# Kernel tuning notes

Hardware: AMD Instinct MI355X
Metric: run time of the kernel (lower is better)

Reference implementation:

```python
import jax, jax.numpy as jnp
import numpy as np

B, N, C, E = 512, 1000, 50, 128
H, D = 8, 16          # head_num, qkv_dim; H*D == E
CLIP = 10.0           # logit_clipping
NEG = -1e9


def setup_inputs() -> dict:
    key = jax.random.key(0)
    ks = jax.random.split(key, 20)
    f = lambda i, shape, s=1.0: jax.random.normal(ks[i], shape, dtype=jnp.float32) * s
    w = 0.05  # small weight scale so tanh/softmax stay in a sane range
    return dict(
        depot_embedding=f(0, (B, 1, E)),
        cluster_embedding=f(1, (B, C, E)),
        current_embedding=f(2, (B, 1, E)),
        node_embeddings=f(3, (B, N, E)),
        aug_context_embedding=f(4, (B, 1, 4 * E)),
        cluster_guidance_embedding=f(5, (B, 1, E)),
        Wq=f(6, (3 * E, E), w), Wk=f(7, (E, E), w), Wv=f(8, (E, E), w), Wks=f(9, (E, E), w),
        mha_Wq=f(10, (E, H * D), w), mha_Wk=f(11, (E, H * D), w),
        mha_Wv=f(12, (E, H * D), w), mha_Wo=f(13, (H * D, E), w),
        is_new_cluster=jax.random.bernoulli(ks[14], 0.5, (B,)),
        mask=jax.random.bernoulli(ks[15], 0.5, (B, 1, N)),
        cluster_mask=jax.random.bernoulli(ks[16], 0.5, (B, 1, N)),
        visited_cluster_mask=jax.random.bernoulli(ks[17], 0.3, (B, 1, C)),
        cluster_guidance=jax.random.randint(ks[18], (B,), 0, C),
        step=1,
    )


def reference(depot_embedding, cluster_embedding, current_embedding, node_embeddings,
              aug_context_embedding, cluster_guidance_embedding,
              Wq, Wk, Wv, Wks, mha_Wq, mha_Wk, mha_Wv, mha_Wo,
              is_new_cluster, mask, cluster_mask, visited_cluster_mask,
              cluster_guidance, step):
    # step > 0 path: init_* buffers come from the passed-in tensors.
    b, n, e = node_embeddings.shape
    c = cluster_embedding.shape[1]

    def unvisit_embed(m):  # m: [B,1,N] bool, True = visited
        mm = m[:, 0, :, None]                                    # [B,N,1]
        return jnp.where(mm, 0.0, node_embeddings).sum(axis=1, keepdims=True) / n  # [B,1,E]

    # --- new-cluster branch, computed full-batch and selected with where ---
    unvisit_mean = unvisit_embed(mask)                            # [B,1,E]
    context = jnp.concatenate([unvisit_mean, current_embedding, depot_embedding], axis=2)  # [B,1,3E]
    q = context @ Wq                                              # [B,1,E]
    k = cluster_embedding @ Wk                                    # [B,C,E]
    v = cluster_embedding @ Wv                                    # [B,C,E]
    pk = cluster_embedding @ Wks                                  # [B,C,E]

    # if all non-depot clusters visited, unmask cluster 0; else mask it
    all_visited = jnp.all(visited_cluster_mask[:, 0, 1:], axis=1)  # [B]
    vcm = visited_cluster_mask.at[:, 0, 0].set(~all_visited)      # [B,1,C]

    # multi-head glimpse attention
    qh = (q @ mha_Wq).reshape(b, 1, H, D).transpose(0, 2, 1, 3)   # [B,H,1,D]
    kh = (k @ mha_Wk).reshape(b, c, H, D).transpose(0, 2, 1, 3)   # [B,H,C,D]
    vh = (v @ mha_Wv).reshape(b, c, H, D).transpose(0, 2, 1, 3)   # [B,H,C,D]
    scores = jnp.einsum('bhqd,bhkd->bhqk', qh, kh) / jnp.sqrt(jnp.float32(D))
    scores = jnp.where(vcm[:, None, :, :], NEG, scores)           # mask over keys
    attn = jax.nn.softmax(scores, axis=-1)
    glimpse = jnp.einsum('bhqk,bhkd->bhqd', attn, vh)             # [B,H,1,D]
    glimpse = glimpse.transpose(0, 2, 1, 3).reshape(b, 1, H * D) @ mha_Wo  # [B,1,E]

    logit = jnp.einsum('bqe,bce->bqc', glimpse, pk)[:, 0, :] / jnp.sqrt(jnp.float32(e))  # [B,C]
    logit = jnp.tanh(logit) * CLIP
    logit = jnp.where(vcm[:, 0, :], NEG, logit)
    log_p = jax.nn.log_softmax(logit, axis=1)                     # [B,C]

    new_guidance = jnp.argmax(log_p, axis=1)                      # greedy select_mode
    new_guid_embed = jnp.take_along_axis(cluster_embedding, new_guidance[:, None, None], axis=1)  # [B,1,E]

    unvisit_cluster = unvisit_embed(mask | cluster_mask)          # [B,1,E]
    new_aug = jnp.concatenate([unvisit_cluster, current_embedding, new_guid_embed, depot_embedding], axis=2)  # [B,1,4E]

    # --- scatter back: keep old values for rows without a new cluster ---
    is_new = is_new_cluster
    sel3 = is_new[:, None, None]
    aug_out = jnp.where(sel3, new_aug, aug_context_embedding)
    guid_embed_out = jnp.where(sel3, new_guid_embed, cluster_guidance_embedding)
    guid_out = jnp.where(is_new, new_guidance.astype(cluster_guidance.dtype), cluster_guidance)
    clu_prob = jnp.where(is_new[:, None], log_p, 0.0)
    return aug_out, guid_embed_out, guid_out, clu_prob
```

## Files before the change

### kernel.cpp

```cpp
#include <hip/hip_runtime.h>
#include <hip/hip_bf16.h>
#include <math.h>

#define BB 512
#define NN 1000
#define CC 50
#define EE 128
#define HH 8
#define DD 16
#define NEGV (-1000000000.0f)

#define O_AUG 0
#define O_GE  (512*512)
#define O_G   (O_GE + 512*128)
#define O_CP  (O_G + 512)

__global__ __launch_bounds__(128) void combine_w(
    const float* __restrict__ Wq, const float* __restrict__ Wk,
    const float* __restrict__ Wv,
    const float* __restrict__ mWq, const float* __restrict__ mWk,
    const float* __restrict__ mWv,
    float* __restrict__ Wqh, float* __restrict__ Wkh, float* __restrict__ Wvh)
{
    int rb = blockIdx.x;
    int e  = threadIdx.x;
    const float* A; const float* Bm; float* O; int r; float scale;
    if (rb < 384)      { A = Wq; Bm = mWq; O = Wqh; r = rb;       scale = 0.25f; }
    else if (rb < 512) { A = Wk; Bm = mWk; O = Wkh; r = rb - 384; scale = 1.0f; }
    else               { A = Wv; Bm = mWv; O = Wvh; r = rb - 512; scale = 1.0f; }
    float acc = 0.0f;
#pragma unroll 8
    for (int i = 0; i < 128; ++i)
        acc = fmaf(A[r * 128 + i], Bm[i * 128 + e], acc);
    O[r * 128 + e] = acc * scale;
}

__global__ __launch_bounds__(512) void reduce_nodes(
    const float* __restrict__ node, const int* __restrict__ mask,
    const int* __restrict__ cmask,
    float* __restrict__ um, float* __restrict__ uc)
{
    int b = blockIdx.x;
    int t = threadIdx.x;
    int v = t & 31;
    int r = t >> 5;

    const float4* np = (const float4*)(node + (long)b * NN * EE);
    const int* mb  = mask  + (long)b * NN;
    const int* cb  = cmask + (long)b * NN;

    float4 a1 = make_float4(0.f, 0.f, 0.f, 0.f);
    float4 a2 = make_float4(0.f, 0.f, 0.f, 0.f);
    for (int n = r; n < NN; n += 16) {
        float4 x = np[n * 32 + v];
        int m1 = mb[n];
        int m2 = m1 | cb[n];
        if (!m1) { a1.x += x.x; a1.y += x.y; a1.z += x.z; a1.w += x.w; }
        if (!m2) { a2.x += x.x; a2.y += x.y; a2.z += x.z; a2.w += x.w; }
    }

    __shared__ float4 s1[16][32];
    __shared__ float4 s2[16][32];
    s1[r][v] = a1;
    s2[r][v] = a2;
    __syncthreads();
    if (t < 128) {
        const float* f1 = (const float*)s1;
        const float* f2 = (const float*)s2;
        float x1 = 0.f, x2 = 0.f;
#pragma unroll
        for (int rr = 0; rr < 16; ++rr) {
            x1 += f1[rr * 128 + t];
            x2 += f2[rr * 128 + t];
        }
        um[b * 128 + t] = x1 * (1.0f / (float)NN);
        uc[b * 128 + t] = x2 * (1.0f / (float)NN);
    }
}

__global__ __launch_bounds__(256) void fused_attn(
    const float* __restrict__ depot, const float* __restrict__ ce,
    const float* __restrict__ cur,   const float* __restrict__ augc,
    const float* __restrict__ cge,
    const int* __restrict__ isnew_p, const int* __restrict__ vmask,
    const int* __restrict__ guid,
    const float* __restrict__ Wks,   const float* __restrict__ Wo,
    const float* __restrict__ um,    const float* __restrict__ uc,
    const float* __restrict__ Wqh,   const float* __restrict__ Wkh,
    const float* __restrict__ Wvh,
    float* __restrict__ out)
{
    int b = blockIdx.x;
    int t = threadIdx.x;

    __shared__ float sT[128 * 57];
    __shared__ float sctx[384];
    __shared__ float sqh[128];
    __shared__ float sU[8 * 128];
    __shared__ float sattn[8 * 64];
    __shared__ float sp[8 * 128];
    __shared__ float sg[128];
    __shared__ float sgo[128];
    __shared__ float sr[128];
    __shared__ float slog[64];
    __shared__ int   svcm[64];
    __shared__ float s_m, s_lse;
    __shared__ int   s_arg;

    const float* ceb = ce + (long)b * CC * EE;

    for (int u = t; u < CC * EE; u += 256) {
        int j = u >> 7, i = u & 127;
        sT[i * 57 + j] = ceb[u];
    }
    if (t < 128) {
        sctx[t]       = um[b * 128 + t];
        sctx[128 + t] = cur[b * 128 + t];
        sctx[256 + t] = depot[b * 128 + t];
    }
    if (t < CC) svcm[t] = vmask[b * CC + t];
    __syncthreads();

    if (t == 0) {
        int allv = 1;
        for (int j = 1; j < CC; ++j) allv &= (svcm[j] != 0);
        svcm[0] = !allv;
    }
    if (t < 128) {
        float acc = 0.f;
#pragma unroll 8
        for (int i = 0; i < 384; ++i)
            acc = fmaf(sctx[i], Wqh[i * 128 + t], acc);
        sqh[t] = acc;
    }
    __syncthreads();

    for (int u = t; u < 8 * 128; u += 256) {
        int h = u >> 7, i = u & 127;
        const float* wk = Wkh + i * 128 + h * 16;
        const float* q  = sqh + h * 16;
        float acc = 0.f;
#pragma unroll
        for (int d = 0; d < 16; ++d) acc = fmaf(wk[d], q[d], acc);
        sU[u] = acc;
    }
    __syncthreads();

    for (int u = t; u < 8 * CC; u += 256) {
        int h = u / CC, j = u - h * CC;
        float acc = 0.f;
#pragma unroll 8
        for (int i = 0; i < 128; ++i)
            acc = fmaf(sT[i * 57 + j], sU[h * 128 + i], acc);
        sattn[h * 64 + j] = svcm[j] ? NEGV : acc;
    }
    __syncthreads();

    if (t < 8) {
        float m = -INFINITY;
        for (int j = 0; j < CC; ++j) m = fmaxf(m, sattn[t * 64 + j]);
        float s = 0.f;
        for (int j = 0; j < CC; ++j) s += expf(sattn[t * 64 + j] - m);
        float inv = 1.0f / s;
        for (int j = 0; j < CC; ++j)
            sattn[t * 64 + j] = expf(sattn[t * 64 + j] - m) * inv;
    }
    __syncthreads();

    for (int u = t; u < 8 * 128; u += 256) {
        int h = u >> 7, i = u & 127;
        float acc = 0.f;
#pragma unroll
        for (int j = 0; j < CC; ++j)
            acc = fmaf(sattn[h * 64 + j], sT[i * 57 + j], acc);
        sp[u] = acc;
    }
    __syncthreads();

    if (t < 128) {
        int h = t >> 4;
        float acc = 0.f;
#pragma unroll 8
        for (int i = 0; i < 128; ++i)
            acc = fmaf(sp[h * 128 + i], Wvh[i * 128 + t], acc);
        sg[t] = acc;
    }
    __syncthreads();

    if (t < 128) {
        float acc = 0.f;
#pragma unroll 8
        for (int i = 0; i < 128; ++i)
            acc = fmaf(sg[i], Wo[i * 128 + t], acc);
        sgo[t] = acc;
    }
    __syncthreads();

    if (t < 128) {
        float acc = 0.f;
#pragma unroll 8
        for (int e = 0; e < 128; ++e)
            acc = fmaf(Wks[t * 128 + e], sgo[e], acc);
        sr[t] = acc;
    }
    __syncthreads();

    if (t < CC) {
        float acc = 0.f;
#pragma unroll 8
        for (int i = 0; i < 128; ++i)
            acc = fmaf(sT[i * 57 + t], sr[i], acc);
        float l = tanhf(acc * 0.08838834764831845f) * 10.0f;
        slog[t] = svcm[t] ? NEGV : l;
    }
    __syncthreads();

    if (t == 0) {
        float m = -INFINITY;
        for (int j = 0; j < CC; ++j) m = fmaxf(m, slog[j]);
        float s = 0.f;
        for (int j = 0; j < CC; ++j) s += expf(slog[j] - m);
        int arg = 0; float best = slog[0];
        for (int j = 1; j < CC; ++j)
            if (slog[j] > best) { best = slog[j]; arg = j; }
        s_m = m; s_lse = logf(s); s_arg = arg;
    }
    __syncthreads();

    bool nw = (isnew_p[b] != 0);
    int  g  = s_arg;
    if (t == 0) {
        out[O_G + b] = nw ? (float)g : (float)guid[b];
    }
    if (t < 128) {
        float nge = sT[t * 57 + g];
        const float* ac = augc + (long)b * 512;
        float a0 = nw ? uc[b * 128 + t]    : ac[t];
        float a1 = nw ? cur[b * 128 + t]   : ac[128 + t];
        float a2 = nw ? nge                : ac[256 + t];
        float a3 = nw ? depot[b * 128 + t] : ac[384 + t];
        float* ao = out + O_AUG + (long)b * 512;
        ao[t] = a0; ao[128 + t] = a1; ao[256 + t] = a2; ao[384 + t] = a3;
        out[O_GE + b * 128 + t] = nw ? nge : cge[b * 128 + t];
    }
    if (t < CC) {
        out[O_CP + b * CC + t] = nw ? ((slog[t] - s_m) - s_lse) : 0.0f;
    }
}

extern "C" void kernel_launch(void* const* d_in, const int* in_sizes, int n_in,
                              void* d_out, int out_size, void* d_ws, size_t ws_size,
                              hipStream_t stream) {
    const float* depot = (const float*)d_in[0];
    const float* ce    = (const float*)d_in[1];
    const float* cur   = (const float*)d_in[2];
    const float* node  = (const float*)d_in[3];
    const float* augc  = (const float*)d_in[4];
    const float* cge   = (const float*)d_in[5];
    const float* Wq    = (const float*)d_in[6];
    const float* Wk    = (const float*)d_in[7];
    const float* Wv    = (const float*)d_in[8];
    const float* Wks   = (const float*)d_in[9];
    const float* mWq   = (const float*)d_in[10];
    const float* mWk   = (const float*)d_in[11];
    const float* mWv   = (const float*)d_in[12];
    const float* mWo   = (const float*)d_in[13];
    const int*   isnew = (const int*)d_in[14];
    const int*   mask  = (const int*)d_in[15];
    const int*   cmask = (const int*)d_in[16];
    const int*   vmask = (const int*)d_in[17];
    const int*   guid  = (const int*)d_in[18];
    float* out = (float*)d_out;

    float* ws  = (float*)d_ws;
    float* um  = ws;
    float* uc  = um  + 512 * 128;
    float* Wqh = uc  + 512 * 128;
    float* Wkh = Wqh + 384 * 128;
    float* Wvh = Wkh + 128 * 128;

    combine_w<<<640, 128, 0, stream>>>(Wq, Wk, Wv, mWq, mWk, mWv, Wqh, Wkh, Wvh);
    reduce_nodes<<<512, 512, 0, stream>>>(node, mask, cmask, um, uc);
    fused_attn<<<512, 256, 0, stream>>>(depot, ce, cur, augc, cge,
                                        isnew, vmask, guid, Wks, mWo,
                                        um, uc, Wqh, Wkh, Wvh, out);
}
```

Baseline: 478.2 us.

## Fuse weight combination into node-reduction kernel, precompute Wo·Wks, warp-shuffle reductions

Merges the weight-combination and node-mean kernels into one launch, with extra blocks computing the combined weights including a new premultiplied Wo·Wks^T matrix. That matrix lets the attention kernel skip one 128x128 matvec stage and one barrier. The node reduction now uses precomputed float mask weights, nontemporal vector loads and 4x unrolling. The serial single-thread softmax, log-softmax and argmax loops become wave-shuffle reductions, and the q projection is split across all 256 threads. The trade-off is an extra workspace buffer and a change in floating-point rounding order.

```diff
diff --git a/kernel.cpp b/kernel.cpp
--- a/kernel.cpp
+++ b/kernel.cpp
@@ -15,66 +15,100 @@
 #define O_G   (O_GE + 512*128)
 #define O_CP  (O_G + 512)
 
-__global__ __launch_bounds__(128) void combine_w(
-    const float* __restrict__ Wq, const float* __restrict__ Wk,
-    const float* __restrict__ Wv,
-    const float* __restrict__ mWq, const float* __restrict__ mWk,
-    const float* __restrict__ mWv,
-    float* __restrict__ Wqh, float* __restrict__ Wkh, float* __restrict__ Wvh)
-{
-    int rb = blockIdx.x;
-    int e  = threadIdx.x;
-    const float* A; const float* Bm; float* O; int r; float scale;
-    if (rb < 384)      { A = Wq; Bm = mWq; O = Wqh; r = rb;       scale = 0.25f; }
-    else if (rb < 512) { A = Wk; Bm = mWk; O = Wkh; r = rb - 384; scale = 1.0f; }
-    else               { A = Wv; Bm = mWv; O = Wvh; r = rb - 512; scale = 1.0f; }
-    float acc = 0.0f;
-#pragma unroll 8
-    for (int i = 0; i < 128; ++i)
-        acc = fmaf(A[r * 128 + i], Bm[i * 128 + e], acc);
-    O[r * 128 + e] = acc * scale;
-}
-
-__global__ __launch_bounds__(512) void reduce_nodes(
+typedef float vf4 __attribute__((ext_vector_type(4)));
+
+__global__ __launch_bounds__(512) void prep(
     const float* __restrict__ node, const int* __restrict__ mask,
     const int* __restrict__ cmask,
-    float* __restrict__ um, float* __restrict__ uc)
+    const float* __restrict__ Wq, const float* __restrict__ Wk,
+    const float* __restrict__ Wv, const float* __restrict__ Wks,
+    const float* __restrict__ mWq, const float* __restrict__ mWk,
+    const float* __restrict__ mWv, const float* __restrict__ Wo,
+    float* __restrict__ um, float* __restrict__ uc,
+    float* __restrict__ Wqh, float* __restrict__ Wkh,
+    float* __restrict__ Wvh, float* __restrict__ WoKs)
 {
-    int b = blockIdx.x;
     int t = threadIdx.x;
-    int v = t & 31;
-    int r = t >> 5;
-
-    const float4* np = (const float4*)(node + (long)b * NN * EE);
-    const int* mb  = mask  + (long)b * NN;
-    const int* cb  = cmask + (long)b * NN;
-
-    float4 a1 = make_float4(0.f, 0.f, 0.f, 0.f);
-    float4 a2 = make_float4(0.f, 0.f, 0.f, 0.f);
-    for (int n = r; n < NN; n += 16) {
-        float4 x = np[n * 32 + v];
-        int m1 = mb[n];
-        int m2 = m1 | cb[n];
-        if (!m1) { a1.x += x.x; a1.y += x.y; a1.z += x.z; a1.w += x.w; }
-        if (!m2) { a2.x += x.x; a2.y += x.y; a2.z += x.z; a2.w += x.w; }
-    }
-
-    __shared__ float4 s1[16][32];
-    __shared__ float4 s2[16][32];
-    s1[r][v] = a1;
-    s2[r][v] = a2;
-    __syncthreads();
-    if (t < 128) {
-        const float* f1 = (const float*)s1;
-        const float* f2 = (const float*)s2;
-        float x1 = 0.f, x2 = 0.f;
-#pragma unroll
-        for (int rr = 0; rr < 16; ++rr) {
-            x1 += f1[rr * 128 + t];
-            x2 += f2[rr * 128 + t];
-        }
-        um[b * 128 + t] = x1 * (1.0f / (float)NN);
-        uc[b * 128 + t] = x2 * (1.0f / (float)NN);
+    if (blockIdx.x < 512) {
+        __shared__ float2 w[1000];
+        __shared__ vf4 s1[16][32];
+        __shared__ vf4 s2[16][32];
+        int b = blockIdx.x;
+        const int* mb = mask  + b * NN;
+        const int* cb = cmask + b * NN;
+        for (int n = t; n < NN; n += 512) {
+            int m1 = mb[n];
+            int m2 = m1 | cb[n];
+            w[n] = make_float2(m1 ? 0.f : 1.f, m2 ? 0.f : 1.f);
+        }
+        __syncthreads();
+
+        int v = t & 31, r = t >> 5;
+        const vf4* np = (const vf4*)(node + (size_t)b * NN * EE);
+        vf4 a1 = {0.f, 0.f, 0.f, 0.f};
+        vf4 a2 = {0.f, 0.f, 0.f, 0.f};
+        int n = r;
+        for (; n + 48 < NN; n += 64) {
+            vf4 x0 = __builtin_nontemporal_load(np + (n     ) * 32 + v);
+            vf4 x1 = __builtin_nontemporal_load(np + (n + 16) * 32 + v);
+            vf4 x2 = __builtin_nontemporal_load(np + (n + 32) * 32 + v);
+            vf4 x3 = __builtin_nontemporal_load(np + (n + 48) * 32 + v);
+            float2 w0 = w[n], w1 = w[n + 16], w2 = w[n + 32], w3 = w[n + 48];
+            a1 += x0 * w0.x; a2 += x0 * w0.y;
+            a1 += x1 * w1.x; a2 += x1 * w1.y;
+            a1 += x2 * w2.x; a2 += x2 * w2.y;
+            a1 += x3 * w3.x; a2 += x3 * w3.y;
+        }
+        for (; n < NN; n += 16) {
+            vf4 x = __builtin_nontemporal_load(np + n * 32 + v);
+            float2 ww = w[n];
+            a1 += x * ww.x;
+            a2 += x * ww.y;
+        }
+        s1[r][v] = a1;
+        s2[r][v] = a2;
+        __syncthreads();
+        if (t < 128) {
+            const float* f1 = (const float*)s1;
+            const float* f2 = (const float*)s2;
+            float x1 = 0.f, x2 = 0.f;
+#pragma unroll
+            for (int rr = 0; rr < 16; ++rr) {
+                x1 += f1[rr * 128 + t];
+                x2 += f2[rr * 128 + t];
+            }
+            um[b * 128 + t] = x1 * (1.0f / (float)NN);
+            uc[b * 128 + t] = x2 * (1.0f / (float)NN);
+        }
+    } else {
+        int wb = blockIdx.x - 512;
+        int r0 = wb * 16;
+        int sub = t >> 7;
+        int e = t & 127;
+        const float* A; const float* Bm; float* O; int rb; float sc; bool tb;
+        if (r0 < 384)      { A = Wq; Bm = mWq; O = Wqh;  rb = r0;       sc = 0.25f; tb = false; }
+        else if (r0 < 512) { A = Wk; Bm = mWk; O = Wkh;  rb = r0 - 384; sc = 1.0f;  tb = false; }
+        else if (r0 < 640) { A = Wv; Bm = mWv; O = Wvh;  rb = r0 - 512; sc = 1.0f;  tb = false; }
+        else               { A = Wo; Bm = Wks; O = WoKs; rb = r0 - 640; sc = 1.0f;  tb = true;  }
+        float acc[4] = {0.f, 0.f, 0.f, 0.f};
+        if (!tb) {
+            for (int i = 0; i < 128; ++i) {
+                float bv = Bm[i * 128 + e];
+#pragma unroll
+                for (int k = 0; k < 4; ++k)
+                    acc[k] = fmaf(A[(rb + sub + 4 * k) * 128 + i], bv, acc[k]);
+            }
+        } else {
+            for (int i = 0; i < 128; ++i) {
+                float bv = Bm[e * 128 + i];
+#pragma unroll
+                for (int k = 0; k < 4; ++k)
+                    acc[k] = fmaf(A[(rb + sub + 4 * k) * 128 + i], bv, acc[k]);
+            }
+        }
+#pragma unroll
+        for (int k = 0; k < 4; ++k)
+            O[(rb + sub + 4 * k) * 128 + e] = acc[k] * sc;
     }
 }
 
@@ -84,10 +118,9 @@
     const float* __restrict__ cge,
     const int* __restrict__ isnew_p, const int* __restrict__ vmask,
     const int* __restrict__ guid,
-    const float* __restrict__ Wks,   const float* __restrict__ Wo,
     const float* __restrict__ um,    const float* __restrict__ uc,
     const float* __restrict__ Wqh,   const float* __restrict__ Wkh,
-    const float* __restrict__ Wvh,
+    const float* __restrict__ Wvh,   const float* __restrict__ WoKs,
     float* __restrict__ out)
 {
     int b = blockIdx.x;
@@ -96,18 +129,18 @@
     __shared__ float sT[128 * 57];
     __shared__ float sctx[384];
     __shared__ float sqh[128];
+    __shared__ float spq[2][128];
     __shared__ float sU[8 * 128];
     __shared__ float sattn[8 * 64];
-    __shared__ float sp[8 * 128];
+    __shared__ float sp[8 * 136];
     __shared__ float sg[128];
-    __shared__ float sgo[128];
     __shared__ float sr[128];
     __shared__ float slog[64];
     __shared__ int   svcm[64];
     __shared__ float s_m, s_lse;
     __shared__ int   s_arg;
 
-    const float* ceb = ce + (long)b * CC * EE;
+    const float* ceb = ce + (size_t)b * CC * EE;
 
     for (int u = t; u < CC * EE; u += 256) {
         int j = u >> 7, i = u & 127;
@@ -118,21 +151,25 @@
         sctx[128 + t] = cur[b * 128 + t];
         sctx[256 + t] = depot[b * 128 + t];
     }
-    if (t < CC) svcm[t] = vmask[b * CC + t];
-    __syncthreads();
-
-    if (t == 0) {
-        int allv = 1;
-        for (int j = 1; j < CC; ++j) allv &= (svcm[j] != 0);
-        svcm[0] = !allv;
-    }
-    if (t < 128) {
-        float acc = 0.f;
-#pragma unroll 8
-        for (int i = 0; i < 384; ++i)
-            acc = fmaf(sctx[i], Wqh[i * 128 + t], acc);
-        sqh[t] = acc;
-    }
+    if (t < 64) svcm[t] = (t < CC) ? vmask[b * CC + t] : 1;
+    __syncthreads();
+
+    if (t < 64) {
+        int pred = (t >= 1 && t < CC) ? (svcm[t] != 0) : 1;
+        int allv = __all(pred);
+        if (t == 0) svcm[0] = !allv;
+    }
+    {
+        int e = t & 127, half = t >> 7;
+        int i0 = half * 192;
+        float acc = 0.f;
+#pragma unroll 8
+        for (int i = 0; i < 192; ++i)
+            acc = fmaf(sctx[i0 + i], Wqh[(i0 + i) * 128 + e], acc);
+        spq[half][e] = acc;
+    }
+    __syncthreads();
+    if (t < 128) sqh[t] = spq[0][t] + spq[1][t];
     __syncthreads();
 
     for (int u = t; u < 8 * 128; u += 256) {
@@ -156,14 +193,23 @@
     }
     __syncthreads();
 
-    if (t < 8) {
-        float m = -INFINITY;
-        for (int j = 0; j < CC; ++j) m = fmaxf(m, sattn[t * 64 + j]);
-        float s = 0.f;
-        for (int j = 0; j < CC; ++j) s += expf(sattn[t * 64 + j] - m);
-        float inv = 1.0f / s;
-        for (int j = 0; j < CC; ++j)
-            sattn[t * 64 + j] = expf(sattn[t * 64 + j] - m) * inv;
+    {
+        int h = t >> 5, l = t & 31;
+        float s0 = sattn[h * 64 + l];
+        float s1v = (l < CC - 32) ? sattn[h * 64 + l + 32] : -INFINITY;
+        float m = fmaxf(s0, s1v);
+#pragma unroll
+        for (int off = 16; off >= 1; off >>= 1)
+            m = fmaxf(m, __shfl_xor(m, off, 32));
+        float e0 = expf(s0 - m);
+        float e1 = (l < CC - 32) ? expf(s1v - m) : 0.f;
+        float ssum = e0 + e1;
+#pragma unroll
+        for (int off = 16; off >= 1; off >>= 1)
+            ssum += __shfl_xor(ssum, off, 32);
+        float inv = 1.0f / ssum;
+        sattn[h * 64 + l] = e0 * inv;
+        if (l < CC - 32) sattn[h * 64 + l + 32] = e1 * inv;
     }
     __syncthreads();
 
@@ -173,7 +219,7 @@
 #pragma unroll
         for (int j = 0; j < CC; ++j)
             acc = fmaf(sattn[h * 64 + j], sT[i * 57 + j], acc);
-        sp[u] = acc;
+        sp[h * 136 + i] = acc;
     }
     __syncthreads();
 
@@ -182,7 +228,7 @@
         float acc = 0.f;
 #pragma unroll 8
         for (int i = 0; i < 128; ++i)
-            acc = fmaf(sp[h * 128 + i], Wvh[i * 128 + t], acc);
+            acc = fmaf(sp[h * 136 + i], Wvh[i * 128 + t], acc);
         sg[t] = acc;
     }
     __syncthreads();
@@ -190,40 +236,41 @@
     if (t < 128) {
         float acc = 0.f;
 #pragma unroll 8
-        for (int i = 0; i < 128; ++i)
-            acc = fmaf(sg[i], Wo[i * 128 + t], acc);
-        sgo[t] = acc;
-    }
-    __syncthreads();
-
-    if (t < 128) {
-        float acc = 0.f;
-#pragma unroll 8
-        for (int e = 0; e < 128; ++e)
-            acc = fmaf(Wks[t * 128 + e], sgo[e], acc);
+        for (int g = 0; g < 128; ++g)
+            acc = fmaf(sg[g], WoKs[g * 128 + t], acc);
         sr[t] = acc;
     }
     __syncthreads();
 
-    if (t < CC) {
-        float acc = 0.f;
-#pragma unroll 8
-        for (int i = 0; i < 128; ++i)
-            acc = fmaf(sT[i * 57 + t], sr[i], acc);
-        float l = tanhf(acc * 0.08838834764831845f) * 10.0f;
-        slog[t] = svcm[t] ? NEGV : l;
-    }
-    __syncthreads();
-
-    if (t == 0) {
-        float m = -INFINITY;
-        for (int j = 0; j < CC; ++j) m = fmaxf(m, slog[j]);
-        float s = 0.f;
-        for (int j = 0; j < CC; ++j) s += expf(slog[j] - m);
-        int arg = 0; float best = slog[0];
-        for (int j = 1; j < CC; ++j)
-            if (slog[j] > best) { best = slog[j]; arg = j; }
-        s_m = m; s_lse = logf(s); s_arg = arg;
+    if (t < 64) {
+        if (t < CC) {
+            float acc = 0.f;
+#pragma unroll 8
+            for (int i = 0; i < 128; ++i)
+                acc = fmaf(sT[i * 57 + t], sr[i], acc);
+            float l = tanhf(acc * 0.08838834764831845f) * 10.0f;
+            slog[t] = svcm[t] ? NEGV : l;
+        } else {
+            slog[t] = NEGV;
+        }
+    }
+    __syncthreads();
+
+    if (t < 64) {
+        float val = (t < CC) ? slog[t] : -INFINITY;
+        int idx = t;
+#pragma unroll
+        for (int off = 32; off >= 1; off >>= 1) {
+            float ov = __shfl_xor(val, off, 64);
+            int   oi = __shfl_xor(idx, off, 64);
+            if (ov > val || (ov == val && oi < idx)) { val = ov; idx = oi; }
+        }
+        float m = val;
+        float ex = (t < CC) ? expf(slog[t] - m) : 0.f;
+#pragma unroll
+        for (int off = 32; off >= 1; off >>= 1)
+            ex += __shfl_xor(ex, off, 64);
+        if (t == 0) { s_m = m; s_arg = idx; s_lse = logf(ex); }
     }
     __syncthreads();
 
@@ -234,12 +281,12 @@
     }
     if (t < 128) {
         float nge = sT[t * 57 + g];
-        const float* ac = augc + (long)b * 512;
+        const float* ac = augc + (size_t)b * 512;
         float a0 = nw ? uc[b * 128 + t]    : ac[t];
         float a1 = nw ? cur[b * 128 + t]   : ac[128 + t];
         float a2 = nw ? nge                : ac[256 + t];
         float a3 = nw ? depot[b * 128 + t] : ac[384 + t];
-        float* ao = out + O_AUG + (long)b * 512;
+        float* ao = out + O_AUG + (size_t)b * 512;
         ao[t] = a0; ao[128 + t] = a1; ao[256 + t] = a2; ao[384 + t] = a3;
         out[O_GE + b * 128 + t] = nw ? nge : cge[b * 128 + t];
     }
@@ -272,16 +319,18 @@
     const int*   guid  = (const int*)d_in[18];
     float* out = (float*)d_out;
 
-    float* ws  = (float*)d_ws;
-    float* um  = ws;
-    float* uc  = um  + 512 * 128;
-    float* Wqh = uc  + 512 * 128;
-    float* Wkh = Wqh + 384 * 128;
-    float* Wvh = Wkh + 128 * 128;
-
-    combine_w<<<640, 128, 0, stream>>>(Wq, Wk, Wv, mWq, mWk, mWv, Wqh, Wkh, Wvh);
-    reduce_nodes<<<512, 512, 0, stream>>>(node, mask, cmask, um, uc);
+    float* ws   = (float*)d_ws;
+    float* um   = ws;
+    float* uc   = um   + 512 * 128;
+    float* Wqh  = uc   + 512 * 128;
+    float* Wkh  = Wqh  + 384 * 128;
+    float* Wvh  = Wkh  + 128 * 128;
+    float* WoKs = Wvh  + 128 * 128;
+
+    prep<<<560, 512, 0, stream>>>(node, mask, cmask,
+                                  Wq, Wk, Wv, Wks, mWq, mWk, mWv, mWo,
+                                  um, uc, Wqh, Wkh, Wvh, WoKs);
     fused_attn<<<512, 256, 0, stream>>>(depot, ce, cur, augc, cge,
-                                        isnew, vmask, guid, Wks, mWo,
-                                        um, uc, Wqh, Wkh, Wvh, out);
+                                        isnew, vmask, guid,
+                                        um, uc, Wqh, Wkh, Wvh, WoKs, out);
 }
```

After: 417.3 us. 12.7% less time.
